# Kernel tuning notes

Hardware: AMD Instinct MI355X
Metric: run time of the kernel (lower is better)

## Reference

```python
import jax, jax.numpy as jnp
import numpy as np

_EPSILON = 1e-06


def _allocation(usage):
    """Freeness-based allocation: sort usage, exclusive cumprod, scatter back.

    usage: [B, M] in [0, 1]. Returns allocation weights [B, M].
    """
    usage = _EPSILON + (1.0 - _EPSILON) * usage
    nonusage = 1.0 - usage
    m = usage.shape[-1]
    sorted_nonusage, indices = jax.lax.top_k(nonusage, k=m)  # descending nonusage = ascending usage
    sorted_usage = 1.0 - sorted_nonusage
    # exclusive cumulative product along the sorted memory axis
    prod_sorted_usage = jnp.concatenate(
        [jnp.ones_like(sorted_usage[:, :1]),
         jnp.cumprod(sorted_usage, axis=1)[:, :-1]], axis=1)
    sorted_allocation = sorted_nonusage * prod_sorted_usage
    # invert the permutation and gather back to original slot order
    inverse_indices = jnp.argsort(indices, axis=1)
    return jnp.take_along_axis(sorted_allocation, inverse_indices, axis=1)


def _updated_usage(write_weights, free_gate, read_weights, prev_usage):
    """Freeness.__call__: usage after write then after read/free. [B, M]."""
    ww = jax.lax.stop_gradient(write_weights)
    # usage after write: increase toward 1 at written slots
    write_w = 1.0 - jnp.prod(1.0 - ww, axis=1)          # [B, M]
    usage = prev_usage + (1.0 - prev_usage) * write_w
    # usage after read: decrease where free_gate*read_weights is high
    free_read = free_gate[:, :, None] * read_weights      # [B, R, M]
    phi = jnp.prod(1.0 - free_read, axis=1)               # [B, M]
    return usage * phi


def _write_allocation_weights(usage, write_gates, num_writes):
    """Per-write-head allocation weights. Returns [B, num_writes, M]."""
    wg = write_gates[:, :, None]                          # [B, W, 1]
    allocs = []
    for i in range(num_writes):  # small fixed head count; sequential by construction
        a = _allocation(usage)
        allocs.append(a)
        usage = usage + (1.0 - usage) * wg[:, i, :] * a
    return jnp.stack(allocs, axis=1)


def setup_inputs() -> dict:
    key = jax.random.key(0)
    ks = jax.random.split(key, 5)
    B, W, R, M = 512, 4, 8, 16384
    return {
        "write_weights": jax.random.uniform(ks[0], (B, W, M), dtype=jnp.float32),
        "free_gate": jax.random.uniform(ks[1], (B, R), dtype=jnp.float32),
        "read_weights": jax.random.uniform(ks[2], (B, R, M), dtype=jnp.float32),
        "prev_usage": jax.random.uniform(ks[3], (B, M), dtype=jnp.float32),
        "write_gates": jax.random.uniform(ks[4], (B, W), dtype=jnp.float32),
        "num_writes": W,
    }


def reference(write_weights, free_gate, read_weights, prev_usage, write_gates, num_writes):
    usage = _updated_usage(write_weights, free_gate, read_weights, prev_usage)
    alloc = _write_allocation_weights(usage, write_gates, num_writes)
    return usage, alloc
```

## Files before the change

kernel.cpp:

```cpp
#include <hip/hip_runtime.h>
#include <stdint.h>

typedef unsigned long long u64;
typedef unsigned int u32;
typedef unsigned short u16;
typedef float f32x4 __attribute__((ext_vector_type(4)));

#define NBINS 512
#define CAP 256
#define POOLCAP 2048
#define LOG_CUT (-64.0f)
#define NT 1024

__device__ __forceinline__ int bucket_of(u32 nnbits) {
    u32 d = 0x3F800000u - nnbits;
    if (d == 0u) d = 1u;
    const int e = 31 - __builtin_clz(d);
    const u32 sub = (e >= 4) ? ((d >> (e - 4)) & 15u) : ((d << (4 - e)) & 15u);
    int v = (e << 4) | (int)sub;
    if (v > NBINS - 1) v = NBINS - 1;
    return (NBINS - 1) - v;
}

__device__ __forceinline__ void nt_store4(float* p, float4 v) {
    f32x4 nv;
    nv.x = v.x; nv.y = v.y; nv.z = v.z; nv.w = v.w;
    __builtin_nontemporal_store(nv, (f32x4*)p);
}

template <int TW, int TR>
__global__ __launch_bounds__(NT, 8)
void fused_kernel(const float* __restrict__ ww,
                  const float* __restrict__ fg,
                  const float* __restrict__ rw,
                  const float* __restrict__ prev,
                  const float* __restrict__ wgt,
                  float* __restrict__ out_usage,
                  float* __restrict__ out_alloc,
                  int B, int W, int R, int M)
{
    __shared__ u64   poolKey[POOLCAP];
    __shared__ float poolLg[POOLCAP];
    __shared__ u64   candKey[CAP];
    __shared__ float candLg[CAP];
    __shared__ u16   candPos[CAP];
    __shared__ u32   hC[NBINS];
    __shared__ float mB[NBINS];
    __shared__ u32   tc[16];
    __shared__ float twv[16];
    __shared__ int   misc[6];

    const int Wl = TW > 0 ? TW : W;
    const int Rl = TR > 0 ? TR : R;
    const int b = blockIdx.x;
    const int t = threadIdx.x;
    const int lane = t & 63;
    const int wid = t >> 6;

    const float C1 = (float)(1.0 - 1e-6);
    const float CE = 1e-6f;
    const size_t rowOff = (size_t)b * M;

    if (t < NBINS) {
        hC[t] = 0u;
        const int v = NBINS - 1 - t;
        const int e = v >> 4;
        const u32 sub = (u32)(v & 15);
        const int sh = e >= 4 ? e - 4 : 0;
        u64 dhi64 = ((u64)(17u + sub) << sh) + 1u;
        u32 dhi = dhi64 > 0x3F800000ull ? 0x3F800000u : (u32)dhi64;
        const float nnlo = __uint_as_float(0x3F800000u - dhi);
        float ueub = 1.0f - nnlo;
        ueub = ueub < 1e-38f ? 1e-38f : (ueub > 0.9999999f ? 0.9999999f : ueub);
        mB[t] = __log2f(ueub);
    }
    if (t == 0) { misc[0] = 0; misc[3] = NBINS; }
    __syncthreads();

    {
        float frs[TR > 0 ? TR : 8];
        #pragma unroll
        for (int r = 0; r < Rl; ++r) frs[r] = fg[(size_t)b * Rl + r];

        const float4 z = make_float4(0.f, 0.f, 0.f, 0.f);
        for (int m = t * 4; m < M; m += NT * 4) {
            const float4 pv = *(const float4*)(prev + rowOff + m);
            float pr0 = 1.f, pr1 = 1.f, pr2 = 1.f, pr3 = 1.f;
            #pragma unroll
            for (int w = 0; w < Wl; ++w) {
                const float4 a = *(const float4*)(ww + ((size_t)b * Wl + w) * M + m);
                pr0 *= (1.0f - a.x); pr1 *= (1.0f - a.y);
                pr2 *= (1.0f - a.z); pr3 *= (1.0f - a.w);
            }
            float u0 = pv.x + (1.0f - pv.x) * (1.0f - pr0);
            float u1 = pv.y + (1.0f - pv.y) * (1.0f - pr1);
            float u2 = pv.z + (1.0f - pv.z) * (1.0f - pr2);
            float u3 = pv.w + (1.0f - pv.w) * (1.0f - pr3);
            float f0 = 1.f, f1 = 1.f, f2 = 1.f, f3 = 1.f;
            #pragma unroll
            for (int r = 0; r < Rl; ++r) {
                const float fr = frs[r];
                const float4 a = *(const float4*)(rw + ((size_t)b * Rl + r) * M + m);
                f0 *= (1.0f - fr * a.x); f1 *= (1.0f - fr * a.y);
                f2 *= (1.0f - fr * a.z); f3 *= (1.0f - fr * a.w);
            }
            float4 uo;
            uo.x = u0 * f0; uo.y = u1 * f1; uo.z = u2 * f2; uo.w = u3 * f3;
            *(float4*)(out_usage + rowOff + m) = uo;
            #pragma unroll
            for (int w = 0; w < Wl; ++w)
                nt_store4(out_alloc + ((size_t)b * Wl + w) * M + m, z);
            const float ua[4] = {uo.x, uo.y, uo.z, uo.w};
            #pragma unroll
            for (int j = 0; j < 4; ++j) {
                const float nn = 1.0f - (CE + C1 * ua[j]);
                atomicAdd(&hC[bucket_of(__float_as_uint(nn))], 1u);
            }
        }
    }
    __syncthreads();

    {
        const bool act = (t < NBINS);
        u32 sc = 0; int x = 0;
        if (act) {
            x = NBINS - 1 - t;
            sc = hC[x];
            #pragma unroll
            for (int off = 1; off < 64; off <<= 1) {
                const u32 oc = __shfl_up(sc, off);
                if (lane >= off) sc += oc;
            }
            if (lane == 63) tc[wid] = sc;
        }
        __syncthreads();
        if (act) {
            u32 ac = 0;
            for (int q = 0; q < wid; ++q) ac += tc[q];
            sc += ac;
            if (sc <= (u32)POOLCAP) atomicMin(&misc[3], x);
        }
    }
    __syncthreads();
    const int pc = misc[3];

    for (int m = t * 4; m < M; m += NT * 4) {
        const float4 uu = *(const float4*)(out_usage + rowOff + m);
        const float ua[4] = {uu.x, uu.y, uu.z, uu.w};
        #pragma unroll
        for (int j = 0; j < 4; ++j) {
            const float ue = CE + C1 * ua[j];
            const float nn = 1.0f - ue;
            const u32 nnbits = __float_as_uint(nn);
            const int bkt = bucket_of(nnbits);
            const bool pred = (bkt >= pc) && (pc < NBINS);
            const u64 mask = __ballot(pred);
            const int cnt = __popcll(mask);
            if (cnt) {
                int base = 0;
                if (lane == 0) base = atomicAdd(&misc[0], cnt);
                base = __shfl(base, 0);
                if (pred) {
                    const int pos = base + __popcll(mask & ((1ull << lane) - 1));
                    if (pos < POOLCAP) {
                        poolKey[pos] = (((u64)(~nnbits)) << 16) | (u64)(u32)(m + j);
                        poolLg[pos] = __log2f(ue);
                    }
                }
            }
        }
    }
    __syncthreads();
    int P = misc[0]; if (P > POOLCAP) P = POOLCAP;

    for (int i = 0; i < Wl; ++i) {
        const float wgi = wgt[(size_t)b * Wl + i];
        float* orow = out_alloc + ((size_t)b * Wl + i) * M;

        if (t == 0) { misc[4] = 0; misc[1] = -1; misc[2] = NBINS; }
        __syncthreads();

        {
            const bool act = (t < NBINS);
            u32 sc = 0; float sw = 0.f; int x = 0;
            if (act) {
                x = NBINS - 1 - t;
                const u32 c = hC[x];
                sc = c;
                sw = mB[x] * (float)c;
                #pragma unroll
                for (int off = 1; off < 64; off <<= 1) {
                    const u32  oc = __shfl_up(sc, off);
                    const float ow = __shfl_up(sw, off);
                    if (lane >= off) { sc += oc; sw += ow; }
                }
                if (lane == 63) { tc[wid] = sc; twv[wid] = sw; }
            }
            __syncthreads();
            if (act) {
                u32 ac = 0; float aw = 0.f;
                for (int q = 0; q < wid; ++q) { ac += tc[q]; aw += twv[q]; }
                sc += ac; sw += aw;
                if (x >= pc) {
                    if (sw <= LOG_CUT) atomicMax(&misc[1], x);
                    if (sc <= (u32)CAP) atomicMin(&misc[2], x);
                }
            }
        }
        __syncthreads();
        const int xs = misc[1];
        const int xc = misc[2];
        const int cut = (xs > xc) ? xs : xc;

        for (int p = t; p < P; p += NT) {
            const u64 key = poolKey[p];
            const u32 nnbits = ~((u32)(key >> 16));
            const int bkt = bucket_of(nnbits);
            const bool pred = (bkt >= cut) && (cut < NBINS);
            const u64 mask = __ballot(pred);
            const int cnt = __popcll(mask);
            if (cnt) {
                int base = 0;
                if (lane == 0) base = atomicAdd(&misc[4], cnt);
                base = __shfl(base, 0);
                if (pred) {
                    const int pos = base + __popcll(mask & ((1ull << lane) - 1));
                    if (pos < CAP) {
                        candKey[pos] = key;
                        candLg[pos] = poolLg[p];
                        candPos[pos] = (u16)p;
                    }
                }
            }
        }
        __syncthreads();
        int K = misc[4]; if (K > CAP) K = CAP;

        if (t < K) {
            const u64 mykey = candKey[t];
            float S = 0.0f;
            #pragma unroll 4
            for (int k = 0; k < K; ++k) {
                const u64 kk = candKey[k];
                const float lg = candLg[k];
                if (kk < mykey) S += lg;
            }
            const u32 nnbits = ~((u32)(mykey >> 16));
            const float nn = __uint_as_float(nnbits);
            const int idx = (int)(mykey & 0xFFFFull);
            const float al = nn * __builtin_exp2f(S);
            if (al != 0.0f) {
                orow[idx] = al;
                if (i + 1 < Wl) {
                    const float u0v = 1.0f - (nn + CE) / C1;
                    const float ucur = (1.0f - nn - CE) / C1;
                    const float unew = ucur + ((1.0f - ucur) * wgi) * al;
                    const float nn2 = 1.0f - (CE + C1 * unew);
                    const u32 nn2bits = __float_as_uint(nn2);
                    const int p = (int)candPos[t];
                    poolKey[p] = (((u64)(~nn2bits)) << 16) | (u64)(u32)idx;
                    poolLg[p] = __log2f(1.0f - nn2);
                    const int bold = bucket_of(nnbits);
                    const int bnew = bucket_of(nn2bits);
                    if (bnew != bold) {
                        atomicSub(&hC[bold], 1u);
                        atomicAdd(&hC[bnew], 1u);
                    }
                }
            }
        }
        __syncthreads();
    }
}

extern "C" void kernel_launch(void* const* d_in, const int* in_sizes, int n_in,
                              void* d_out, int out_size, void* d_ws, size_t ws_size,
                              hipStream_t stream) {
    const float* ww   = (const float*)d_in[0];
    const float* fg   = (const float*)d_in[1];
    const float* rw   = (const float*)d_in[2];
    const float* prev = (const float*)d_in[3];
    const float* wgt  = (const float*)d_in[4];
    const int BWM = in_sizes[0];
    const int BR  = in_sizes[1];
    const int BM  = in_sizes[3];
    const int BW  = in_sizes[4];
    const int M = BWM / BW;
    const int B = BM / M;
    const int W = BW / B;
    const int R = BR / B;

    float* out_usage = (float*)d_out;
    float* out_alloc = out_usage + (size_t)BM;

    if (W == 4 && R == 8) {
        hipLaunchKernelGGL((fused_kernel<4, 8>), dim3(B), dim3(NT), 0, stream,
                           ww, fg, rw, prev, wgt, out_usage, out_alloc, B, W, R, M);
    } else {
        hipLaunchKernelGGL((fused_kernel<0, 0>), dim3(B), dim3(NT), 0, stream,
                           ww, fg, rw, prev, wgt, out_usage, out_alloc, B, W, R, M);
    }
}
```

Measured before the change: 146.4 us.

## Buffer sparse allocation results in LDS bitmaps and write alloc rows once

Instead of zero-filling the whole allocation output up front and then scattering the nonzero values into global memory, each head records its nonzero slots in a shared-memory bitmap with prefix offsets and a compact value array. At the end, one dense pass writes every allocation row with nontemporal float4 stores, filling in the stored values. This removes the scattered global writes and avoids the ordering between the zero fill and the scatter. The cost is more LDS, extra barriers and prefix-scan work per head, and the specialized path now requires M == 16384.

```diff
diff --git a/kernel.cpp b/kernel.cpp
--- a/kernel.cpp
+++ b/kernel.cpp
@@ -11,6 +11,7 @@
 #define POOLCAP 2048
 #define LOG_CUT (-64.0f)
 #define NT 1024
+#define MWW 256
 
 __device__ __forceinline__ int bucket_of(u32 nnbits) {
     u32 d = 0x3F800000u - nnbits;
@@ -49,6 +50,9 @@
     __shared__ u32   tc[16];
     __shared__ float twv[16];
     __shared__ int   misc[6];
+    __shared__ u64   bmS[TW > 0 ? TW : 1][MWW];
+    __shared__ u32   boS[TW > 0 ? TW : 1][MWW];
+    __shared__ float valS[TW > 0 ? TW : 1][CAP];
 
     const int Wl = TW > 0 ? TW : W;
     const int Rl = TR > 0 ? TR : R;
@@ -74,6 +78,7 @@
         ueub = ueub < 1e-38f ? 1e-38f : (ueub > 0.9999999f ? 0.9999999f : ueub);
         mB[t] = __log2f(ueub);
     }
+    if (TW > 0 && t < TW * MWW) bmS[t >> 8][t & (MWW - 1)] = 0ull;
     if (t == 0) { misc[0] = 0; misc[3] = NBINS; }
     __syncthreads();
 
@@ -82,7 +87,6 @@
         #pragma unroll
         for (int r = 0; r < Rl; ++r) frs[r] = fg[(size_t)b * Rl + r];
 
-        const float4 z = make_float4(0.f, 0.f, 0.f, 0.f);
         for (int m = t * 4; m < M; m += NT * 4) {
             const float4 pv = *(const float4*)(prev + rowOff + m);
             float pr0 = 1.f, pr1 = 1.f, pr2 = 1.f, pr3 = 1.f;
@@ -107,9 +111,11 @@
             float4 uo;
             uo.x = u0 * f0; uo.y = u1 * f1; uo.z = u2 * f2; uo.w = u3 * f3;
             *(float4*)(out_usage + rowOff + m) = uo;
-            #pragma unroll
-            for (int w = 0; w < Wl; ++w)
-                nt_store4(out_alloc + ((size_t)b * Wl + w) * M + m, z);
+            if (TW == 0) {
+                const float4 z = make_float4(0.f, 0.f, 0.f, 0.f);
+                for (int w = 0; w < Wl; ++w)
+                    nt_store4(out_alloc + ((size_t)b * Wl + w) * M + m, z);
+            }
             const float ua[4] = {uo.x, uo.y, uo.z, uo.w};
             #pragma unroll
             for (int j = 0; j < 4; ++j) {
@@ -236,6 +242,7 @@
         __syncthreads();
         int K = misc[4]; if (K > CAP) K = CAP;
 
+        float myAl = 0.0f; int myIdx = -1;
         if (t < K) {
             const u64 mykey = candKey[t];
             float S = 0.0f;
@@ -250,9 +257,13 @@
             const int idx = (int)(mykey & 0xFFFFull);
             const float al = nn * __builtin_exp2f(S);
             if (al != 0.0f) {
-                orow[idx] = al;
+                if (TW > 0) {
+                    myAl = al; myIdx = idx;
+                    atomicOr(&bmS[i][idx >> 6], 1ull << (idx & 63));
+                } else {
+                    orow[idx] = al;
+                }
                 if (i + 1 < Wl) {
-                    const float u0v = 1.0f - (nn + CE) / C1;
                     const float ucur = (1.0f - nn - CE) / C1;
                     const float unew = ucur + ((1.0f - ucur) * wgi) * al;
                     const float nn2 = 1.0f - (CE + C1 * unew);
@@ -269,7 +280,56 @@
                 }
             }
         }
-        __syncthreads();
+        if (TW > 0) {
+            __syncthreads();
+            u32 myinc = 0, mycnt = 0;
+            if (t < MWW) {
+                mycnt = (u32)__popcll(bmS[i][t]);
+                myinc = mycnt;
+                #pragma unroll
+                for (int off = 1; off < 64; off <<= 1) {
+                    const u32 o = __shfl_up(myinc, off);
+                    if (lane >= off) myinc += o;
+                }
+                if (lane == 63) tc[wid] = myinc;
+            }
+            __syncthreads();
+            if (t < MWW) {
+                u32 add = 0;
+                for (int q = 0; q < wid; ++q) add += tc[q];
+                boS[i][t] = myinc + add - mycnt;
+            }
+            __syncthreads();
+            if (myIdx >= 0) {
+                const u64 wb = bmS[i][myIdx >> 6];
+                const int xr = (int)boS[i][myIdx >> 6]
+                             + (int)__popcll(wb & ((1ull << (myIdx & 63)) - 1));
+                valS[i][xr] = myAl;
+            }
+        }
+        __syncthreads();
+    }
+
+    if (TW > 0) {
+        for (int m4 = t * 4; m4 < M; m4 += NT * 4) {
+            const int word = m4 >> 6;
+            const int bit0 = m4 & 63;
+            #pragma unroll
+            for (int w = 0; w < TW; ++w) {
+                const u64 wb = bmS[w][word];
+                float4 o = make_float4(0.f, 0.f, 0.f, 0.f);
+                if ((wb >> bit0) & 15ull) {
+                    int base = (int)boS[w][word]
+                             + (int)__popcll(wb & ((1ull << bit0) - 1));
+                    float* op = &o.x;
+                    #pragma unroll
+                    for (int j = 0; j < 4; ++j) {
+                        if ((wb >> (bit0 + j)) & 1ull) op[j] = valS[w][base++];
+                    }
+                }
+                nt_store4(out_alloc + ((size_t)b * TW + w) * M + m4, o);
+            }
+        }
     }
 }
 
@@ -293,7 +353,7 @@
     float* out_usage = (float*)d_out;
     float* out_alloc = out_usage + (size_t)BM;
 
-    if (W == 4 && R == 8) {
+    if (W == 4 && R == 8 && M == 16384) {
         hipLaunchKernelGGL((fused_kernel<4, 8>), dim3(B), dim3(NT), 0, stream,
                            ww, fg, rw, prev, wgt, out_usage, out_alloc, B, W, R, M);
     } else {
```

Measured after the change: 146.6 us. No clear change (+0.1%).
